# Kernel optimization log

Hardware: AMD Instinct MI355X
Metric: run time of the kernel (lower is better)

Reference implementation:

```python
import jax, jax.numpy as jnp
import numpy as np

GROUPS = 32
EPS = 1e-6


def group_norm(x, gamma, beta):
    b, c, h, w = x.shape
    xg = x.reshape(b, GROUPS, c // GROUPS, h, w)
    mu = xg.mean(axis=(2, 3, 4), keepdims=True)
    var = xg.var(axis=(2, 3, 4), keepdims=True)
    xn = ((xg - mu) * jax.lax.rsqrt(var + EPS)).reshape(b, c, h, w)
    return xn * gamma[None, :, None, None] + beta[None, :, None, None]


def conv1x1(x, w, b):
    # x: (b,c_in,h,w), w: (c_out,c_in), b: (c_out,)
    return jnp.einsum('oc,bchw->bohw', w, x) + b[None, :, None, None]


def setup_inputs() -> dict:
    key = jax.random.key(0)
    ks = jax.random.split(key, 10)
    c = 512
    scale = 1.0 / np.sqrt(c)
    inp = jax.random.normal(ks[0], (16, c, 32, 32), dtype=jnp.float32)
    return {
        'inp': inp,
        'gamma': jnp.ones((c,), jnp.float32),
        'beta': jnp.zeros((c,), jnp.float32),
        'Wq': jax.random.normal(ks[1], (c, c), jnp.float32) * scale,
        'bq': jnp.zeros((c,), jnp.float32),
        'Wk': jax.random.normal(ks[2], (c, c), jnp.float32) * scale,
        'bk': jnp.zeros((c,), jnp.float32),
        'Wv': jax.random.normal(ks[3], (c, c), jnp.float32) * scale,
        'bv': jnp.zeros((c,), jnp.float32),
        'Wo': jax.random.normal(ks[4], (c, c), jnp.float32) * scale,
        'bo': jnp.zeros((c,), jnp.float32),
    }


def reference(inp, gamma, beta, Wq, bq, Wk, bk, Wv, bv, Wo, bo):
    b, c, h, w = inp.shape
    x = group_norm(inp, gamma, beta)
    Q = conv1x1(x, Wq, bq).reshape(b, c, h * w)  # (b,c,n)
    K = conv1x1(x, Wk, bk).reshape(b, c, h * w)  # (b,c,m)
    V = conv1x1(x, Wv, bv).reshape(b, c, h * w)  # (b,c,m)
    # attn[b,n,m] = sum_c Q[b,c,n] * K[b,c,m], scaled then softmax over m
    attn = jnp.einsum('bcn,bcm->bnm', Q, K) / jnp.sqrt(jnp.float32(c))
    attn = jax.nn.softmax(attn, axis=2)
    # A[b,c,n] = sum_m V[b,c,m] * attn[b,n,m]  (== bmm(V, attn^T))
    A = jnp.einsum('bcm,bnm->bcn', V, attn).reshape(b, c, h, w)
    A = conv1x1(A, Wo, bo)
    return inp + A
```

## Files before the change

kernel.cpp:

```cpp
#include <hip/hip_runtime.h>

typedef unsigned short UST;
typedef __attribute__((ext_vector_type(8))) short bf16x8;
typedef __attribute__((ext_vector_type(8))) unsigned short us8;
typedef __attribute__((ext_vector_type(4))) float f32x4;

__device__ __forceinline__ UST f2bf(float f) {
  union { float f; unsigned int u; } x; x.f = f;
  unsigned int r = x.u + 0x7fffu + ((x.u >> 16) & 1u);
  return (UST)(r >> 16);
}
__device__ __forceinline__ float bf2f(UST h) {
  union { unsigned int u; float f; } x; x.u = ((unsigned int)h) << 16;
  return x.f;
}

__device__ __forceinline__ void sync_lds() {
  asm volatile("s_waitcnt lgkmcnt(0)\n\ts_barrier" ::: "memory");
}
__device__ __forceinline__ void barrier_nowait() {
  asm volatile("s_barrier" ::: "memory");
}

typedef const __attribute__((address_space(1))) void g_void;
typedef __attribute__((address_space(3))) void lds_void;
__device__ __forceinline__ void gload16(const UST* g, UST* l) {
  __builtin_amdgcn_global_load_lds((g_void*)g, (lds_void*)l, 16, 0, 0);
}

__global__ __launch_bounds__(256) void prep(
    const float* __restrict__ inp, const float* __restrict__ gamma,
    const float* __restrict__ beta, UST* __restrict__ Xnt,
    const float4* __restrict__ wq, const float4* __restrict__ wk,
    const float4* __restrict__ wv, const float4* __restrict__ wo,
    ushort4* __restrict__ oqkv, ushort4* __restrict__ owo,
    const float4* __restrict__ bq4, const float4* __restrict__ bk4,
    const float4* __restrict__ bv4, float4* __restrict__ bqkv4,
    float4* __restrict__ l4) {
  const int tid = threadIdx.x;
  if (blockIdx.x >= 768) {
    int i = (blockIdx.x - 768) * 256 + tid;
    l4[i] = make_float4(0.f, 0.f, 0.f, 0.f);
    return;
  }
  if (blockIdx.x >= 512) {
    const int wb = blockIdx.x - 512;
    int i = wb * 256 + tid;
    float4 v;
    v = wq[i]; oqkv[i]          = make_ushort4(f2bf(v.x), f2bf(v.y), f2bf(v.z), f2bf(v.w));
    v = wk[i]; oqkv[i + 65536]  = make_ushort4(f2bf(v.x), f2bf(v.y), f2bf(v.z), f2bf(v.w));
    v = wv[i]; oqkv[i + 131072] = make_ushort4(f2bf(v.x), f2bf(v.y), f2bf(v.z), f2bf(v.w));
    v = wo[i]; owo[i]           = make_ushort4(f2bf(v.x), f2bf(v.y), f2bf(v.z), f2bf(v.w));
    if (wb < 2) {
      int t = wb * 256 + tid;
      if (t < 384) bqkv4[t] = (t < 128) ? bq4[t] : (t < 256 ? bk4[t - 128] : bv4[t - 256]);
    }
    return;
  }
  const int g = blockIdx.x & 31, b = blockIdx.x >> 5;
  const float4* p4 = (const float4*)(inp + ((size_t)b * 32 + g) * 16384);
  float x[16][4];
  float s = 0.f, ss = 0.f;
#pragma unroll
  for (int i = 0; i < 16; i++) {
    float4 t = p4[tid + i * 256];
    x[i][0] = t.x; x[i][1] = t.y; x[i][2] = t.z; x[i][3] = t.w;
    s += t.x + t.y + t.z + t.w;
    ss += t.x * t.x + t.y * t.y + t.z * t.z + t.w * t.w;
  }
  for (int o = 32; o >= 1; o >>= 1) { s += __shfl_xor(s, o); ss += __shfl_xor(ss, o); }
  __shared__ float red[8];
  __shared__ float mu_s, rstd_s;
  const int w = tid >> 6;
  if ((tid & 63) == 0) { red[w * 2] = s; red[w * 2 + 1] = ss; }
  __syncthreads();
  if (tid == 0) {
    float S1 = red[0] + red[2] + red[4] + red[6];
    float S2 = red[1] + red[3] + red[5] + red[7];
    float mu = S1 * (1.f / 16384.f);
    float var = S2 * (1.f / 16384.f) - mu * mu;
    mu_s = mu; rstd_s = rsqrtf(var + 1e-6f);
  }
  __syncthreads();
  const float mu = mu_s, rstd = rstd_s;
#pragma unroll
  for (int o2 = 0; o2 < 2; o2++) {
    const int ccg = g * 2 + o2;
    float sc[8], sh[8];
#pragma unroll
    for (int j = 0; j < 8; j++) {
      int ch = ccg * 8 + j;
      sc[j] = gamma[ch] * rstd;
      sh[j] = beta[ch] - mu * sc[j];
    }
#pragma unroll
    for (int m = 0; m < 4; m++) {
      us8 v;
#pragma unroll
      for (int j = 0; j < 8; j++) v[j] = f2bf(x[o2 * 8 + j][m] * sc[j] + sh[j]);
      *(us8*)(Xnt + (size_t)b * 524288 + (size_t)ccg * 8192 + (size_t)(4 * tid + m) * 8) = v;
    }
  }
}

template <int EPI, int NT, int AR, int BR>
__global__ __launch_bounds__(256, 4) void gemm_bt(
    const UST* __restrict__ A, const UST* __restrict__ B, void* __restrict__ C,
    const float* __restrict__ bias, const float* __restrict__ extra, float scale,
    int K, int ldc,
    int rsA, int csA, int ssA, int rsB, int csB, int ssB,
    long zA, long zB, long zC) {
  __shared__ __align__(16) UST buf[16384];

  const int tid = threadIdx.x;
  int m0, n0, z;
  if constexpr (NT > 0) {
    int lin = blockIdx.x + NT * (blockIdx.y + gridDim.y * blockIdx.z);
    int T = gridDim.y * gridDim.z;
    int per = T >> 3;
    int g = lin & 7, idx = lin >> 3;
    int at = g * per + idx / NT;
    int x = idx % NT;
    m0 = (at % gridDim.y) * 128; z = at / gridDim.y; n0 = x * 128;
  } else {
    m0 = blockIdx.y * 128; n0 = blockIdx.x * 128; z = blockIdx.z;
  }
  const UST* Ab = A + (long)z * zA;
  const UST* Bb = B + (long)z * zB;

  const int w = tid >> 6, lane = tid & 63;
  const int quad = lane >> 4, l16 = lane & 15;
  const int wm = w >> 1, wn = w & 1;

  f32x4 acc[4][4];
#pragma unroll
  for (int i = 0; i < 4; i++)
#pragma unroll
    for (int j = 0; j < 4; j++) acc[i][j] = f32x4{0.f, 0.f, 0.f, 0.f};

  const UST* gA[2];
  const UST* gB[2];
#pragma unroll
  for (int t = 0; t < 2; t++) {
    int q = t * 256 + w * 64 + lane;
    int row, kc;
    if constexpr (AR) { kc = q >> 7; row = q & 127; }
    else {
      row = q >> 2; int kk = q & 3;
      kc = kk ^ (((row >> 1) ^ (row >> 3)) & 3);
    }
    gA[t] = Ab + (size_t)(m0 + row) * rsA + (size_t)kc * csA;
  }
#pragma unroll
  for (int t = 0; t < 2; t++) {
    int q = t * 256 + w * 64 + lane;
    int row, kc;
    if constexpr (BR) { kc = q >> 7; row = q & 127; }
    else {
      row = q >> 2; int kk = q & 3;
      kc = kk ^ (((row >> 1) ^ (row >> 3)) & 3);
    }
    gB[t] = Bb + (size_t)(n0 + row) * rsB + (size_t)kc * csB;
  }
  int aoff[4], boff[4];
#pragma unroll
  for (int i = 0; i < 4; i++) {
    int R = wm * 64 + i * 16 + l16;
    if constexpr (AR) aoff[i] = quad * 1024 + R * 8;
    else {
      int s = ((R >> 1) ^ (R >> 3)) & 3;
      aoff[i] = R * 32 + (quad ^ s) * 8;
    }
  }
#pragma unroll
  for (int j = 0; j < 4; j++) {
    int R = wn * 64 + j * 16 + l16;
    if constexpr (BR) boff[j] = quad * 1024 + R * 8;
    else {
      int s = ((R >> 1) ^ (R >> 3)) & 3;
      boff[j] = R * 32 + (quad ^ s) * 8;
    }
  }

  const int nk = K >> 5;

#define STAGE(bb)                                   \
  {                                                 \
    UST* sA = buf + (bb) * 8192;                    \
    UST* sB = sA + 4096;                            \
    _Pragma("unroll") for (int t = 0; t < 2; t++) { \
      gload16(gA[t], sA + t * 2048 + w * 512);      \
      gA[t] += ssA;                                 \
    }                                               \
    _Pragma("unroll") for (int t = 0; t < 2; t++) { \
      gload16(gB[t], sB + t * 2048 + w * 512);      \
      gB[t] += ssB;                                 \
    }                                               \
  }

  STAGE(0)
  STAGE(1)

  for (int k = 0; k < nk; ++k) {
    if (k + 1 < nk) asm volatile("s_waitcnt vmcnt(4)" ::: "memory");
    else            asm volatile("s_waitcnt vmcnt(0)" ::: "memory");
    barrier_nowait();
    const UST* cA = buf + (k & 1) * 8192;
    const UST* cB = cA + 4096;
    bf16x8 af[4], bfr[4];
#pragma unroll
    for (int i = 0; i < 4; i++) af[i] = *(const bf16x8*)(cA + aoff[i]);
#pragma unroll
    for (int j = 0; j < 4; j++) bfr[j] = *(const bf16x8*)(cB + boff[j]);
    __builtin_amdgcn_s_setprio(1);
#pragma unroll
    for (int i = 0; i < 4; i++)
#pragma unroll
      for (int j = 0; j < 4; j++)
        acc[i][j] = __builtin_amdgcn_mfma_f32_16x16x32_bf16(af[i], bfr[j], acc[i][j], 0, 0, 0);
    __builtin_amdgcn_s_setprio(0);
    if (k + 2 < nk) {
      sync_lds();
      STAGE(k & 1)
    }
  }
  sync_lds();

  if constexpr (EPI == 4) {
    float* fbuf = (float*)buf;
    float* Cb = (float*)C + (long)z * zC;
    const float* Eb = extra + (long)z * zC;
#pragma unroll
    for (int p = 0; p < 4; ++p) {
      if (p) barrier_nowait();
      if (wm == (p >> 1)) {
#pragma unroll
        for (int ii = 0; ii < 2; ii++) {
          const int i = (p & 1) * 2 + ii;
#pragma unroll
          for (int j = 0; j < 4; j++)
#pragma unroll
            for (int r = 0; r < 4; r++)
              fbuf[(ii * 16 + quad * 4 + r) * 132 + wn * 64 + j * 16 + l16] = acc[i][j][r];
        }
      }
      sync_lds();
#pragma unroll
      for (int it = 0; it < 4; ++it) {
        int q = tid + it * 256;
        int row = q >> 5, colc = q & 31;
        int gr = m0 + p * 32 + row;
        size_t off = (size_t)gr * ldc + n0 + colc * 4;
        float4 v = *(float4*)&fbuf[row * 132 + colc * 4];
        float4 e = *(const float4*)&Eb[off];
        float bb = bias[gr];
        v.x += bb + e.x; v.y += bb + e.y; v.z += bb + e.z; v.w += bb + e.w;
        *(float4*)&Cb[off] = v;
      }
    }
  } else if constexpr (EPI == 7) {
    UST* Cb = (UST*)C + (long)z * zC;
    float* lrow = (float*)extra + (long)z * 1024;
#pragma unroll
    for (int h = 0; h < 2; ++h) {
      if (h) barrier_nowait();
      if (wm == h) {
#pragma unroll
        for (int i = 0; i < 4; i++)
#pragma unroll
          for (int j = 0; j < 4; j++)
#pragma unroll
            for (int r = 0; r < 4; r++) {
              float v = __expf(acc[i][j][r] * scale);
              buf[(i * 16 + quad * 4 + r) * 136 + wn * 64 + j * 16 + l16] = f2bf(v);
            }
      }
      sync_lds();
#pragma unroll
      for (int it = 0; it < 4; ++it) {
        int q = tid + it * 256;
        int row = q >> 4, colc = q & 15;
        us8 v = *(us8*)&buf[row * 136 + colc * 8];
        *(us8*)&Cb[(size_t)(m0 + h * 64 + row) * ldc + n0 + colc * 8] = v;
        float s = 0.f;
#pragma unroll
        for (int j = 0; j < 8; j++) s += bf2f(v[j]);
        s += __shfl_xor(s, 8); s += __shfl_xor(s, 4);
        s += __shfl_xor(s, 2); s += __shfl_xor(s, 1);
        if ((lane & 15) == 0) atomicAdd(&lrow[m0 + h * 64 + row], s);
      }
    }
  } else if constexpr (EPI == 8) {
    UST* Cb = (UST*)C + (long)z * zC;
    const float* lrow = bias + (long)z * 1024;
#pragma unroll
    for (int h = 0; h < 2; ++h) {
      if (h) barrier_nowait();
      if (wm == h) {
#pragma unroll
        for (int i = 0; i < 4; i++) {
          float rs[4];
#pragma unroll
          for (int r = 0; r < 4; r++)
            rs[r] = 1.0f / lrow[m0 + h * 64 + i * 16 + quad * 4 + r];
#pragma unroll
          for (int j = 0; j < 4; j++)
#pragma unroll
            for (int r = 0; r < 4; r++)
              buf[(i * 16 + quad * 4 + r) * 136 + wn * 64 + j * 16 + l16] =
                  f2bf(acc[i][j][r] * rs[r]);
        }
      }
      sync_lds();
#pragma unroll
      for (int it = 0; it < 4; ++it) {
        int q = tid + it * 256;
        int row = q >> 4, colc = q & 15;
        us8 v = *(us8*)&buf[row * 136 + colc * 8];
        *(us8*)&Cb[(size_t)(m0 + h * 64 + row) * ldc + n0 + colc * 8] = v;
      }
    }
  } else {
    const bool vreg = (n0 >= 1024);
    if (!vreg) {
      UST* Cb = (UST*)C + (long)z * zC;
#pragma unroll
      for (int h = 0; h < 2; ++h) {
        if (h) barrier_nowait();
        if (wm == h) {
#pragma unroll
          for (int i = 0; i < 4; i++)
#pragma unroll
            for (int j = 0; j < 4; j++) {
              const float bc = bias[n0 + wn * 64 + j * 16 + l16];
#pragma unroll
              for (int r = 0; r < 4; r++)
                buf[(i * 16 + quad * 4 + r) * 136 + wn * 64 + j * 16 + l16] =
                    f2bf(acc[i][j][r] + bc);
            }
        }
        sync_lds();
#pragma unroll
        for (int it = 0; it < 4; ++it) {
          int q = tid + it * 256;
          int row = q >> 4, colc = q & 15;
          us8 v = *(us8*)&buf[row * 136 + colc * 8];
          *(us8*)&Cb[(size_t)(m0 + h * 64 + row) * ldc + n0 + colc * 8] = v;
        }
      }
    } else {
      UST* Vb = (UST*)extra + (long)z * 524288;
#pragma unroll
      for (int h = 0; h < 2; ++h) {
        if (h) barrier_nowait();
        if (wn == h) {
#pragma unroll
          for (int i = 0; i < 4; i++)
#pragma unroll
            for (int j = 0; j < 4; j++) {
              const float bc = bias[n0 + wn * 64 + j * 16 + l16];
              ushort4 sv;
              sv.x = f2bf(acc[i][j][0] + bc);
              sv.y = f2bf(acc[i][j][1] + bc);
              sv.z = f2bf(acc[i][j][2] + bc);
              sv.w = f2bf(acc[i][j][3] + bc);
              *(ushort4*)&buf[(j * 16 + l16) * 136 + wm * 64 + i * 16 + quad * 4] = sv;
            }
        }
        sync_lds();
#pragma unroll
        for (int it = 0; it < 4; ++it) {
          int q = tid + it * 256;
          int c = q >> 4, mc = q & 15;
          us8 v = *(us8*)&buf[c * 136 + mc * 8];
          *(us8*)&Vb[(size_t)(n0 - 1024 + h * 64 + c) * 1024 + m0 + mc * 8] = v;
        }
      }
    }
  }
#undef STAGE
}

extern "C" void kernel_launch(void* const* d_in, const int* in_sizes, int n_in,
                              void* d_out, int out_size, void* d_ws, size_t ws_size,
                              hipStream_t stream) {
  const float* inp   = (const float*)d_in[0];
  const float* gamma = (const float*)d_in[1];
  const float* beta  = (const float*)d_in[2];
  const float* Wq    = (const float*)d_in[3];
  const float* bq    = (const float*)d_in[4];
  const float* Wk    = (const float*)d_in[5];
  const float* bk    = (const float*)d_in[6];
  const float* Wv    = (const float*)d_in[7];
  const float* bv    = (const float*)d_in[8];
  const float* Wo    = (const float*)d_in[9];
  const float* bo    = (const float*)d_in[10];
  float* out = (float*)d_out;
  char* ws = (char*)d_ws;

  UST*   Xnt   = (UST*)(ws);
  UST*   QKt   = (UST*)(ws + ((size_t)16 << 20));
  UST*   V     = (UST*)(ws + ((size_t)48 << 20));
  UST*   P     = (UST*)(ws + ((size_t)64 << 20));
  float* bqkv  = (float*)(ws + ((size_t)96 << 20));
  UST*   Wqkvb = (UST*)(ws + ((size_t)96 << 20) + 8192);
  UST*   Wob   = Wqkvb + 786432;
  float* l     = (float*)(ws + ((size_t)100 << 20));
  UST*   At    = Xnt;

  prep<<<784, 256, 0, stream>>>(
      inp, gamma, beta, Xnt,
      (const float4*)Wq, (const float4*)Wk, (const float4*)Wv, (const float4*)Wo,
      (ushort4*)Wqkvb, (ushort4*)Wob,
      (const float4*)bq, (const float4*)bk, (const float4*)bv, (float4*)bqkv,
      (float4*)l);

  gemm_bt<6, 12, 1, 0><<<dim3(12, 8, 16), 256, 0, stream>>>(
      Xnt, Wqkvb, QKt, bqkv, (const float*)V, 1.f,
      512, 1024, 8, 8192, 32768, 512, 8, 32, 524288, 0, 1048576);
  gemm_bt<7, 8, 0, 0><<<dim3(8, 8, 16), 256, 0, stream>>>(
      QKt, QKt + 512, P, nullptr, (const float*)l, 0.04419417382415922f,
      512, 1024, 1024, 8, 32, 1024, 8, 32, 1048576, 1048576, 1048576);
  gemm_bt<8, 4, 0, 0><<<dim3(4, 8, 16), 256, 0, stream>>>(
      P, V, At, (const float*)l, nullptr, 1.f,
      1024, 512, 1024, 8, 32, 1024, 8, 32, 1048576, 524288, 524288);
  gemm_bt<4, 8, 0, 0><<<dim3(8, 4, 16), 256, 0, stream>>>(
      Wob, At, out, bo, inp, 1.f,
      512, 1024, 512, 8, 32, 512, 8, 32, 0, 524288, 524288);
}
```

Measured before the change: 213.4 us.

## Add 256x256-tile 8-wave GEMM with phased prefetch for QKV and QK^T

Adds a new gemm8p kernel: 512 threads, 256x256 output tiles, a 128 KB double-buffered LDS and a four-phase ping-pong schedule. In each phase, MFMA work overlaps the global-to-LDS staging of the next K slice, with explicit vmcnt waits and setprio. The QKV projection and the exp(QK^T) score GEMM now use it, with their epilogues moved over; the gemm_bt variants lose those epilogues. The larger tiles are meant to raise data reuse per loaded byte and hide load latency. In exchange, fewer blocks are launched (384 and 256) and register/LDS pressure is high, which limits occupancy.

```diff
diff --git a/kernel.cpp b/kernel.cpp
--- a/kernel.cpp
+++ b/kernel.cpp
@@ -103,6 +103,233 @@
   }
 }
 
+template <int EPI, int NT, int AR>
+__global__ __launch_bounds__(512, 2) void gemm8p(
+    const UST* __restrict__ A, const UST* __restrict__ B, void* __restrict__ C,
+    const float* __restrict__ bias, const float* __restrict__ extra, float scale,
+    int K, int ldc, int rsA, int csA, long ssA, int rsB, long ssB,
+    long zA, long zB, long zC) {
+  __shared__ __align__(16) UST buf[65536];
+
+  const int tid = threadIdx.x;
+  int lin = blockIdx.x + NT * (blockIdx.y + gridDim.y * blockIdx.z);
+  int T = gridDim.y * gridDim.z;
+  int per = T >> 3;
+  int g = lin & 7, idx = lin >> 3;
+  int at = g * per + idx / NT;
+  int x = idx % NT;
+  const int m0 = (at % gridDim.y) * 256;
+  const int z = at / gridDim.y;
+  const int n0 = x * 256;
+
+  const UST* Ab = A + (long)z * zA;
+  const UST* Bb = B + (long)z * zB;
+
+  const int w = tid >> 6, lane = tid & 63;
+  const int quad = lane >> 4, l16 = lane & 15;
+  const int wr = w >> 2, wc = w & 3;
+
+  f32x4 acc[8][4];
+#pragma unroll
+  for (int i = 0; i < 8; i++)
+#pragma unroll
+    for (int j = 0; j < 4; j++) acc[i][j] = f32x4{0.f, 0.f, 0.f, 0.f};
+
+  const UST* gp[8];
+  int lo[8];
+  {
+    const int lr = w * 8 + (lane >> 3);
+    const int kcl = (lane & 7) ^ (lane >> 3);
+#pragma unroll
+    for (int p = 0; p < 8; p++) {
+      int q;
+      bool isA;
+      if (p == 0) { q = 0; isA = true; }
+      else if (p == 1) { q = 2; isA = true; }
+      else if (p == 6) { q = 1; isA = true; }
+      else if (p == 7) { q = 3; isA = true; }
+      else { q = p - 2; isA = false; }
+      if (isA) {
+        if (AR) gp[p] = Ab + (size_t)(m0 + q * 64 + lane) * rsA + (size_t)w * csA;
+        else    gp[p] = Ab + (size_t)(m0 + q * 64 + lr) * rsA + (size_t)kcl * csA;
+        lo[p] = q * 4096 + w * 512;
+      } else {
+        gp[p] = Bb + (size_t)(n0 + q * 64 + lr) * rsB + (size_t)kcl * 8;
+        lo[p] = 16384 + q * 4096 + w * 512;
+      }
+    }
+  }
+
+  int aoffs[8][2], boffs[4][2];
+#pragma unroll
+  for (int i = 0; i < 8; i++) {
+    int R = wr * 128 + i * 16 + l16;
+    int q = R >> 6, lr = R & 63;
+#pragma unroll
+    for (int ks = 0; ks < 2; ks++) {
+      int kc = ks * 4 + quad;
+      aoffs[i][ks] = AR ? (q * 4096 + (kc * 64 + lr) * 8)
+                        : (q * 4096 + (lr * 8 + (kc ^ (lr & 7))) * 8);
+    }
+  }
+#pragma unroll
+  for (int j = 0; j < 4; j++) {
+    int R = wc * 64 + j * 16 + l16;
+    int q = R >> 6, lr = R & 63;
+#pragma unroll
+    for (int ks = 0; ks < 2; ks++) {
+      int kc = ks * 4 + quad;
+      boffs[j][ks] = 16384 + q * 4096 + (lr * 8 + (kc ^ (lr & 7))) * 8;
+    }
+  }
+
+  const int nk = K >> 6;
+
+#define STG(P, SS) { gload16(gp[P], lb + lo[P]); gp[P] += (SS); }
+
+  {
+    UST* lb = buf;
+    STG(0, ssA) STG(1, ssA) STG(2, ssB) STG(3, ssB)
+    STG(4, ssB) STG(5, ssB) STG(6, ssA) STG(7, ssA)
+  }
+  asm volatile("s_waitcnt vmcnt(2)" ::: "memory");
+  barrier_nowait();
+
+#define PH(IH, JH, P0, P1, SS0, SS1, VME)                                     \
+  {                                                                           \
+    bf16x8 af[4][2], bfr[2][2];                                               \
+    _Pragma("unroll") for (int il = 0; il < 4; il++)                          \
+      _Pragma("unroll") for (int ks = 0; ks < 2; ks++)                        \
+        af[il][ks] = *(const bf16x8*)(cb + aoffs[(IH)*4 + il][ks]);           \
+    _Pragma("unroll") for (int jl = 0; jl < 2; jl++)                          \
+      _Pragma("unroll") for (int ks = 0; ks < 2; ks++)                        \
+        bfr[jl][ks] = *(const bf16x8*)(cb + boffs[(JH)*2 + jl][ks]);          \
+    if (stg) { STG(P0, SS0) STG(P1, SS1) }                                    \
+    barrier_nowait();                                                         \
+    asm volatile("s_waitcnt lgkmcnt(0)" ::: "memory");                        \
+    __builtin_amdgcn_sched_barrier(0);                                        \
+    __builtin_amdgcn_s_setprio(1);                                            \
+    _Pragma("unroll") for (int il = 0; il < 4; il++)                          \
+      _Pragma("unroll") for (int jl = 0; jl < 2; jl++)                        \
+        _Pragma("unroll") for (int ks = 0; ks < 2; ks++)                      \
+          acc[(IH)*4 + il][(JH)*2 + jl] = __builtin_amdgcn_mfma_f32_16x16x32_bf16( \
+              af[il][ks], bfr[jl][ks], acc[(IH)*4 + il][(JH)*2 + jl], 0, 0, 0);    \
+    __builtin_amdgcn_s_setprio(0);                                            \
+    VME;                                                                      \
+    barrier_nowait();                                                         \
+  }
+
+  for (int t = 0; t < nk; ++t) {
+    const UST* cb = buf + (t & 1) * 32768;
+    UST* lb = buf + ((t + 1) & 1) * 32768;
+    const bool stg = (t + 1 < nk);
+    PH(0, 0, 0, 1, ssA, ssA, {})
+    PH(0, 1, 2, 3, ssB, ssB, {
+      if (stg) { asm volatile("s_waitcnt vmcnt(4)" ::: "memory"); }
+      else     { asm volatile("s_waitcnt vmcnt(0)" ::: "memory"); }
+    })
+    PH(1, 0, 4, 5, ssB, ssB, {})
+    PH(1, 1, 6, 7, ssA, ssA, {
+      if (stg) { asm volatile("s_waitcnt vmcnt(2)" ::: "memory"); }
+    })
+  }
+#undef PH
+#undef STG
+
+  if constexpr (EPI == 7) {
+    UST* Cb = (UST*)C + (long)z * zC;
+    float* lrow = (float*)extra + (long)z * 1024;
+#pragma unroll
+    for (int h = 0; h < 2; ++h) {
+      if (h) barrier_nowait();
+      if (wr == h) {
+#pragma unroll
+        for (int i = 0; i < 8; i++)
+#pragma unroll
+          for (int j = 0; j < 4; j++)
+#pragma unroll
+            for (int r = 0; r < 4; r++) {
+              float v = __expf(acc[i][j][r] * scale);
+              buf[(i * 16 + quad * 4 + r) * 260 + wc * 64 + j * 16 + l16] = f2bf(v);
+            }
+      }
+      sync_lds();
+#pragma unroll
+      for (int it = 0; it < 8; ++it) {
+        int q = tid + it * 512;
+        int row = q >> 5, colc = q & 31;
+        us8 v = *(us8*)&buf[row * 260 + colc * 8];
+        *(us8*)&Cb[(size_t)(m0 + h * 128 + row) * ldc + n0 + colc * 8] = v;
+        float s = 0.f;
+#pragma unroll
+        for (int jj = 0; jj < 8; jj++) s += bf2f(v[jj]);
+        s += __shfl_xor(s, 16); s += __shfl_xor(s, 8);
+        s += __shfl_xor(s, 4); s += __shfl_xor(s, 2); s += __shfl_xor(s, 1);
+        if ((lane & 31) == 0) atomicAdd(&lrow[m0 + h * 128 + row], s);
+      }
+    }
+  } else {
+    const bool vreg = (n0 >= 1024);
+    if (!vreg) {
+      UST* Cb = (UST*)C + (long)z * zC;
+#pragma unroll
+      for (int h = 0; h < 2; ++h) {
+        if (h) barrier_nowait();
+        if (wr == h) {
+#pragma unroll
+          for (int i = 0; i < 8; i++)
+#pragma unroll
+            for (int j = 0; j < 4; j++) {
+              const float bc = bias[n0 + wc * 64 + j * 16 + l16];
+#pragma unroll
+              for (int r = 0; r < 4; r++)
+                buf[(i * 16 + quad * 4 + r) * 260 + wc * 64 + j * 16 + l16] =
+                    f2bf(acc[i][j][r] + bc);
+            }
+        }
+        sync_lds();
+#pragma unroll
+        for (int it = 0; it < 8; ++it) {
+          int q = tid + it * 512;
+          int row = q >> 5, colc = q & 31;
+          us8 v = *(us8*)&buf[row * 260 + colc * 8];
+          *(us8*)&Cb[(size_t)(m0 + h * 128 + row) * ldc + n0 + colc * 8] = v;
+        }
+      }
+    } else {
+      UST* Vb = (UST*)extra + (long)z * 524288;
+#pragma unroll
+      for (int h = 0; h < 2; ++h) {
+        if (h) barrier_nowait();
+        if ((wc >> 1) == h) {
+#pragma unroll
+          for (int i = 0; i < 8; i++)
+#pragma unroll
+            for (int j = 0; j < 4; j++) {
+              const float bc = bias[n0 + wc * 64 + j * 16 + l16];
+              const int Cl = (wc & 1) * 64 + j * 16 + l16;
+              const int R0 = wr * 128 + i * 16 + quad * 4;
+              ushort4 sv;
+              sv.x = f2bf(acc[i][j][0] + bc);
+              sv.y = f2bf(acc[i][j][1] + bc);
+              sv.z = f2bf(acc[i][j][2] + bc);
+              sv.w = f2bf(acc[i][j][3] + bc);
+              *(ushort4*)&buf[Cl * 260 + R0] = sv;
+            }
+        }
+        sync_lds();
+#pragma unroll
+        for (int it = 0; it < 8; ++it) {
+          int q = tid + it * 512;
+          int Cl = q >> 5, mc = q & 31;
+          us8 v = *(us8*)&buf[Cl * 260 + mc * 8];
+          *(us8*)&Vb[(size_t)(n0 - 1024 + h * 128 + Cl) * 1024 + m0 + mc * 8] = v;
+        }
+      }
+    }
+  }
+}
+
 template <int EPI, int NT, int AR, int BR>
 __global__ __launch_bounds__(256, 4) void gemm_bt(
     const UST* __restrict__ A, const UST* __restrict__ B, void* __restrict__ C,
@@ -258,22 +485,26 @@
         *(float4*)&Cb[off] = v;
       }
     }
-  } else if constexpr (EPI == 7) {
+  } else if constexpr (EPI == 8) {
     UST* Cb = (UST*)C + (long)z * zC;
-    float* lrow = (float*)extra + (long)z * 1024;
+    const float* lrow = bias + (long)z * 1024;
 #pragma unroll
     for (int h = 0; h < 2; ++h) {
       if (h) barrier_nowait();
       if (wm == h) {
 #pragma unroll
-        for (int i = 0; i < 4; i++)
+        for (int i = 0; i < 4; i++) {
+          float rs[4];
+#pragma unroll
+          for (int r = 0; r < 4; r++)
+            rs[r] = 1.0f / lrow[m0 + h * 64 + i * 16 + quad * 4 + r];
 #pragma unroll
           for (int j = 0; j < 4; j++)
 #pragma unroll
-            for (int r = 0; r < 4; r++) {
-              float v = __expf(acc[i][j][r] * scale);
-              buf[(i * 16 + quad * 4 + r) * 136 + wn * 64 + j * 16 + l16] = f2bf(v);
-            }
+            for (int r = 0; r < 4; r++)
+              buf[(i * 16 + quad * 4 + r) * 136 + wn * 64 + j * 16 + l16] =
+                  f2bf(acc[i][j][r] * rs[r]);
+        }
       }
       sync_lds();
 #pragma unroll
@@ -282,99 +513,6 @@
         int row = q >> 4, colc = q & 15;
         us8 v = *(us8*)&buf[row * 136 + colc * 8];
         *(us8*)&Cb[(size_t)(m0 + h * 64 + row) * ldc + n0 + colc * 8] = v;
-        float s = 0.f;
-#pragma unroll
-        for (int j = 0; j < 8; j++) s += bf2f(v[j]);
-        s += __shfl_xor(s, 8); s += __shfl_xor(s, 4);
-        s += __shfl_xor(s, 2); s += __shfl_xor(s, 1);
-        if ((lane & 15) == 0) atomicAdd(&lrow[m0 + h * 64 + row], s);
-      }
-    }
-  } else if constexpr (EPI == 8) {
-    UST* Cb = (UST*)C + (long)z * zC;
-    const float* lrow = bias + (long)z * 1024;
-#pragma unroll
-    for (int h = 0; h < 2; ++h) {
-      if (h) barrier_nowait();
-      if (wm == h) {
-#pragma unroll
-        for (int i = 0; i < 4; i++) {
-          float rs[4];
-#pragma unroll
-          for (int r = 0; r < 4; r++)
-            rs[r] = 1.0f / lrow[m0 + h * 64 + i * 16 + quad * 4 + r];
-#pragma unroll
-          for (int j = 0; j < 4; j++)
-#pragma unroll
-            for (int r = 0; r < 4; r++)
-              buf[(i * 16 + quad * 4 + r) * 136 + wn * 64 + j * 16 + l16] =
-                  f2bf(acc[i][j][r] * rs[r]);
-        }
-      }
-      sync_lds();
-#pragma unroll
-      for (int it = 0; it < 4; ++it) {
-        int q = tid + it * 256;
-        int row = q >> 4, colc = q & 15;
-        us8 v = *(us8*)&buf[row * 136 + colc * 8];
-        *(us8*)&Cb[(size_t)(m0 + h * 64 + row) * ldc + n0 + colc * 8] = v;
-      }
-    }
-  } else {
-    const bool vreg = (n0 >= 1024);
-    if (!vreg) {
-      UST* Cb = (UST*)C + (long)z * zC;
-#pragma unroll
-      for (int h = 0; h < 2; ++h) {
-        if (h) barrier_nowait();
-        if (wm == h) {
-#pragma unroll
-          for (int i = 0; i < 4; i++)
-#pragma unroll
-            for (int j = 0; j < 4; j++) {
-              const float bc = bias[n0 + wn * 64 + j * 16 + l16];
-#pragma unroll
-              for (int r = 0; r < 4; r++)
-                buf[(i * 16 + quad * 4 + r) * 136 + wn * 64 + j * 16 + l16] =
-                    f2bf(acc[i][j][r] + bc);
-            }
-        }
-        sync_lds();
-#pragma unroll
-        for (int it = 0; it < 4; ++it) {
-          int q = tid + it * 256;
-          int row = q >> 4, colc = q & 15;
-          us8 v = *(us8*)&buf[row * 136 + colc * 8];
-          *(us8*)&Cb[(size_t)(m0 + h * 64 + row) * ldc + n0 + colc * 8] = v;
-        }
-      }
-    } else {
-      UST* Vb = (UST*)extra + (long)z * 524288;
-#pragma unroll
-      for (int h = 0; h < 2; ++h) {
-        if (h) barrier_nowait();
-        if (wn == h) {
-#pragma unroll
-          for (int i = 0; i < 4; i++)
-#pragma unroll
-            for (int j = 0; j < 4; j++) {
-              const float bc = bias[n0 + wn * 64 + j * 16 + l16];
-              ushort4 sv;
-              sv.x = f2bf(acc[i][j][0] + bc);
-              sv.y = f2bf(acc[i][j][1] + bc);
-              sv.z = f2bf(acc[i][j][2] + bc);
-              sv.w = f2bf(acc[i][j][3] + bc);
-              *(ushort4*)&buf[(j * 16 + l16) * 136 + wm * 64 + i * 16 + quad * 4] = sv;
-            }
-        }
-        sync_lds();
-#pragma unroll
-        for (int it = 0; it < 4; ++it) {
-          int q = tid + it * 256;
-          int c = q >> 4, mc = q & 15;
-          us8 v = *(us8*)&buf[c * 136 + mc * 8];
-          *(us8*)&Vb[(size_t)(n0 - 1024 + h * 64 + c) * 1024 + m0 + mc * 8] = v;
-        }
       }
     }
   }
@@ -415,12 +553,12 @@
       (const float4*)bq, (const float4*)bk, (const float4*)bv, (float4*)bqkv,
       (float4*)l);
 
-  gemm_bt<6, 12, 1, 0><<<dim3(12, 8, 16), 256, 0, stream>>>(
+  gemm8p<6, 6, 1><<<dim3(6, 4, 16), 512, 0, stream>>>(
       Xnt, Wqkvb, QKt, bqkv, (const float*)V, 1.f,
-      512, 1024, 8, 8192, 32768, 512, 8, 32, 524288, 0, 1048576);
-  gemm_bt<7, 8, 0, 0><<<dim3(8, 8, 16), 256, 0, stream>>>(
+      512, 1024, 8, 8192, 65536, 512, 64, 524288, 0, 1048576);
+  gemm8p<7, 4, 0><<<dim3(4, 4, 16), 512, 0, stream>>>(
       QKt, QKt + 512, P, nullptr, (const float*)l, 0.04419417382415922f,
-      512, 1024, 1024, 8, 32, 1024, 8, 32, 1048576, 1048576, 1048576);
+      512, 1024, 1024, 8, 64, 1024, 64, 1048576, 1048576, 1048576);
   gemm_bt<8, 4, 0, 0><<<dim3(4, 8, 16), 256, 0, stream>>>(
       P, V, At, (const float*)l, nullptr, 1.f,
       1024, 512, 1024, 8, 32, 1024, 8, 32, 1048576, 524288, 524288);
```

Result: slower. 241.1 us (+13.0%).

## Fuse QK^T softmax and PV into one attention kernel with P kept in LDS

Applied to the files above, without the earlier changes.

Replaces the separate QK^T+exp GEMM and the P·V GEMM with a single attention kernel. Each 512-thread block computes exp scores for 64 queries against all 1024 keys, keeps the bf16 probabilities in 128KB of shared memory and reduces the row sums locally. It then multiplies by V and normalizes. This removes the global P buffer round trip, the atomicAdd row-sum reduction and the zeroing of l in prep. The cost is a large LDS footprint that limits residency to one block per CU, and Q/K/V operands are loaded straight from global memory without LDS staging, which may expose memory latency.

```diff
diff --git a/kernel.cpp b/kernel.cpp
--- a/kernel.cpp
+++ b/kernel.cpp
@@ -35,14 +35,8 @@
     const float4* __restrict__ wv, const float4* __restrict__ wo,
     ushort4* __restrict__ oqkv, ushort4* __restrict__ owo,
     const float4* __restrict__ bq4, const float4* __restrict__ bk4,
-    const float4* __restrict__ bv4, float4* __restrict__ bqkv4,
-    float4* __restrict__ l4) {
+    const float4* __restrict__ bv4, float4* __restrict__ bqkv4) {
   const int tid = threadIdx.x;
-  if (blockIdx.x >= 768) {
-    int i = (blockIdx.x - 768) * 256 + tid;
-    l4[i] = make_float4(0.f, 0.f, 0.f, 0.f);
-    return;
-  }
   if (blockIdx.x >= 512) {
     const int wb = blockIdx.x - 512;
     int i = wb * 256 + tid;
@@ -103,6 +97,177 @@
   }
 }
 
+__global__ __launch_bounds__(512, 2) void attn(
+    const UST* __restrict__ QKt, const UST* __restrict__ V,
+    UST* __restrict__ At, float scale) {
+  __shared__ __align__(16) UST Ps[65536];
+  __shared__ float lbuf[512];
+  __shared__ __align__(16) float linv[64];
+
+  const int tid = threadIdx.x;
+  const int lin = blockIdx.x;
+  const int b  = (lin & 7) * 2 + (lin >> 7);
+  const int n0 = ((lin >> 3) & 15) * 64;
+
+  const UST* qk = QKt + (size_t)b * 1048576;
+  const UST* vb = V   + (size_t)b * 524288;
+  UST* ob       = At  + (size_t)b * 524288 + (size_t)n0 * 512;
+
+  const int w = tid >> 6, lane = tid & 63;
+  const int quad = lane >> 4, l16 = lane & 15;
+  const int xr = (l16 & 7) << 2;
+
+  int qoff[4];
+#pragma unroll
+  for (int jn = 0; jn < 4; jn++)
+    qoff[jn] = (n0 + jn * 16 + l16) * 1024 + quad * 8;
+
+  float lp[4] = {0.f, 0.f, 0.f, 0.f};
+
+#define LDS1(KF, QF, KS)                                          \
+  _Pragma("unroll") for (int t = 0; t < 4; t++) {                 \
+    KF[t] = *(const bf16x8*)(qk + koff[t] + (KS) * 32);           \
+    QF[t] = *(const bf16x8*)(qk + qoff[t] + (KS) * 32);           \
+  }
+#define MM1(KF, QF)                                               \
+  __builtin_amdgcn_s_setprio(1);                                  \
+  _Pragma("unroll") for (int im = 0; im < 4; im++)                \
+    _Pragma("unroll") for (int jn = 0; jn < 4; jn++)              \
+      s[im][jn] = __builtin_amdgcn_mfma_f32_16x16x32_bf16(        \
+          KF[im], QF[jn], s[im][jn], 0, 0, 0);                    \
+  __builtin_amdgcn_s_setprio(0);
+
+#pragma unroll
+  for (int mg = 0; mg < 2; ++mg) {
+    int koff[4];
+#pragma unroll
+    for (int im = 0; im < 4; im++)
+      koff[im] = (w * 128 + mg * 64 + im * 16 + l16) * 1024 + 512 + quad * 8;
+
+    f32x4 s[4][4];
+#pragma unroll
+    for (int i = 0; i < 4; i++)
+#pragma unroll
+      for (int j = 0; j < 4; j++) s[i][j] = f32x4{0.f, 0.f, 0.f, 0.f};
+
+    bf16x8 kA[4], qA[4], kB[4], qB[4];
+    LDS1(kA, qA, 0)
+#pragma unroll
+    for (int ks2 = 0; ks2 < 8; ks2++) {
+      LDS1(kB, qB, 2 * ks2 + 1)
+      MM1(kA, qA)
+      if (ks2 < 7) { LDS1(kA, qA, 2 * ks2 + 2) }
+      MM1(kB, qB)
+    }
+
+#pragma unroll
+    for (int im = 0; im < 4; im++) {
+      const int chunk = w * 16 + mg * 8 + im * 2 + (quad >> 1);
+#pragma unroll
+      for (int jn = 0; jn < 4; jn++) {
+        ushort4 pv;
+        float e0 = __expf(s[im][jn][0] * scale);
+        float e1 = __expf(s[im][jn][1] * scale);
+        float e2 = __expf(s[im][jn][2] * scale);
+        float e3 = __expf(s[im][jn][3] * scale);
+        pv.x = f2bf(e0); pv.y = f2bf(e1); pv.z = f2bf(e2); pv.w = f2bf(e3);
+        lp[jn] += bf2f(pv.x) + bf2f(pv.y) + bf2f(pv.z) + bf2f(pv.w);
+        const int nl = jn * 16 + l16;
+        *(ushort4*)&Ps[nl * 1024 + (chunk ^ xr) * 8 + (quad & 1) * 4] = pv;
+      }
+    }
+  }
+#undef LDS1
+#undef MM1
+
+#pragma unroll
+  for (int jn = 0; jn < 4; jn++) {
+    lp[jn] += __shfl_xor(lp[jn], 16);
+    lp[jn] += __shfl_xor(lp[jn], 32);
+  }
+  if (quad == 0) {
+#pragma unroll
+    for (int jn = 0; jn < 4; jn++) lbuf[w * 64 + jn * 16 + l16] = lp[jn];
+  }
+  sync_lds();
+  if (tid < 64) {
+    float sa = 0.f;
+#pragma unroll
+    for (int ww = 0; ww < 8; ww++) sa += lbuf[ww * 64 + tid];
+    linv[tid] = 1.0f / sa;
+  }
+  sync_lds();
+
+  f32x4 o[4][4];
+#pragma unroll
+  for (int i = 0; i < 4; i++)
+#pragma unroll
+    for (int j = 0; j < 4; j++) o[i][j] = f32x4{0.f, 0.f, 0.f, 0.f};
+
+  int voff[4];
+#pragma unroll
+  for (int jc = 0; jc < 4; jc++)
+    voff[jc] = (w * 64 + jc * 16 + l16) * 1024 + quad * 8;
+  int pbase[4];
+#pragma unroll
+  for (int i = 0; i < 4; i++) pbase[i] = (i * 16 + l16) * 1024;
+
+#define LDV(VF, KS)                                               \
+  _Pragma("unroll") for (int t = 0; t < 4; t++)                   \
+    VF[t] = *(const bf16x8*)(vb + voff[t] + (KS) * 32);
+#define LDP(PF, KS)                                               \
+  _Pragma("unroll") for (int t = 0; t < 4; t++)                   \
+    PF[t] = *(const bf16x8*)&Ps[pbase[t] + ((((KS) * 4 + quad) ^ xr) << 3)];
+#define MM2(PF, VF)                                               \
+  __builtin_amdgcn_s_setprio(1);                                  \
+  _Pragma("unroll") for (int i = 0; i < 4; i++)                   \
+    _Pragma("unroll") for (int jc = 0; jc < 4; jc++)              \
+      o[i][jc] = __builtin_amdgcn_mfma_f32_16x16x32_bf16(         \
+          PF[i], VF[jc], o[i][jc], 0, 0, 0);                      \
+  __builtin_amdgcn_s_setprio(0);
+
+  {
+    bf16x8 vA[4], vB[4];
+    LDV(vA, 0)
+#pragma unroll
+    for (int ks2 = 0; ks2 < 16; ks2++) {
+      bf16x8 pA[4], pB[4];
+      LDP(pA, 2 * ks2)
+      LDV(vB, 2 * ks2 + 1)
+      MM2(pA, vA)
+      LDP(pB, 2 * ks2 + 1)
+      if (ks2 < 15) { LDV(vA, 2 * ks2 + 2) }
+      MM2(pB, vB)
+    }
+  }
+#undef LDV
+#undef LDP
+#undef MM2
+
+  sync_lds();
+  f32x4 li[4];
+#pragma unroll
+  for (int i = 0; i < 4; i++) li[i] = *(f32x4*)&linv[i * 16 + quad * 4];
+
+  UST* obuf = Ps;
+#pragma unroll
+  for (int i = 0; i < 4; i++)
+#pragma unroll
+    for (int jc = 0; jc < 4; jc++)
+#pragma unroll
+      for (int r = 0; r < 4; r++)
+        obuf[(i * 16 + quad * 4 + r) * 520 + w * 64 + jc * 16 + l16] =
+            f2bf(o[i][jc][r] * li[i][r]);
+  sync_lds();
+#pragma unroll
+  for (int it = 0; it < 8; ++it) {
+    int q = tid + it * 512;
+    int row = q >> 6, cc = q & 63;
+    us8 vv = *(us8*)&obuf[row * 520 + cc * 8];
+    *(us8*)&ob[(size_t)row * 512 + cc * 8] = vv;
+  }
+}
+
 template <int EPI, int NT, int AR, int BR>
 __global__ __launch_bounds__(256, 4) void gemm_bt(
     const UST* __restrict__ A, const UST* __restrict__ B, void* __restrict__ C,
@@ -256,68 +421,6 @@
         float bb = bias[gr];
         v.x += bb + e.x; v.y += bb + e.y; v.z += bb + e.z; v.w += bb + e.w;
         *(float4*)&Cb[off] = v;
-      }
-    }
-  } else if constexpr (EPI == 7) {
-    UST* Cb = (UST*)C + (long)z * zC;
-    float* lrow = (float*)extra + (long)z * 1024;
-#pragma unroll
-    for (int h = 0; h < 2; ++h) {
-      if (h) barrier_nowait();
-      if (wm == h) {
-#pragma unroll
-        for (int i = 0; i < 4; i++)
-#pragma unroll
-          for (int j = 0; j < 4; j++)
-#pragma unroll
-            for (int r = 0; r < 4; r++) {
-              float v = __expf(acc[i][j][r] * scale);
-              buf[(i * 16 + quad * 4 + r) * 136 + wn * 64 + j * 16 + l16] = f2bf(v);
-            }
-      }
-      sync_lds();
-#pragma unroll
-      for (int it = 0; it < 4; ++it) {
-        int q = tid + it * 256;
-        int row = q >> 4, colc = q & 15;
-        us8 v = *(us8*)&buf[row * 136 + colc * 8];
-        *(us8*)&Cb[(size_t)(m0 + h * 64 + row) * ldc + n0 + colc * 8] = v;
-        float s = 0.f;
-#pragma unroll
-        for (int j = 0; j < 8; j++) s += bf2f(v[j]);
-        s += __shfl_xor(s, 8); s += __shfl_xor(s, 4);
-        s += __shfl_xor(s, 2); s += __shfl_xor(s, 1);
-        if ((lane & 15) == 0) atomicAdd(&lrow[m0 + h * 64 + row], s);
-      }
-    }
-  } else if constexpr (EPI == 8) {
-    UST* Cb = (UST*)C + (long)z * zC;
-    const float* lrow = bias + (long)z * 1024;
-#pragma unroll
-    for (int h = 0; h < 2; ++h) {
-      if (h) barrier_nowait();
-      if (wm == h) {
-#pragma unroll
-        for (int i = 0; i < 4; i++) {
-          float rs[4];
-#pragma unroll
-          for (int r = 0; r < 4; r++)
-            rs[r] = 1.0f / lrow[m0 + h * 64 + i * 16 + quad * 4 + r];
-#pragma unroll
-          for (int j = 0; j < 4; j++)
-#pragma unroll
-            for (int r = 0; r < 4; r++)
-              buf[(i * 16 + quad * 4 + r) * 136 + wn * 64 + j * 16 + l16] =
-                  f2bf(acc[i][j][r] * rs[r]);
-        }
-      }
-      sync_lds();
-#pragma unroll
-      for (int it = 0; it < 4; ++it) {
-        int q = tid + it * 256;
-        int row = q >> 4, colc = q & 15;
-        us8 v = *(us8*)&buf[row * 136 + colc * 8];
-        *(us8*)&Cb[(size_t)(m0 + h * 64 + row) * ldc + n0 + colc * 8] = v;
       }
     }
   } else {
@@ -401,29 +504,21 @@
   UST*   Xnt   = (UST*)(ws);
   UST*   QKt   = (UST*)(ws + ((size_t)16 << 20));
   UST*   V     = (UST*)(ws + ((size_t)48 << 20));
-  UST*   P     = (UST*)(ws + ((size_t)64 << 20));
   float* bqkv  = (float*)(ws + ((size_t)96 << 20));
   UST*   Wqkvb = (UST*)(ws + ((size_t)96 << 20) + 8192);
   UST*   Wob   = Wqkvb + 786432;
-  float* l     = (float*)(ws + ((size_t)100 << 20));
   UST*   At    = Xnt;
 
-  prep<<<784, 256, 0, stream>>>(
+  prep<<<768, 256, 0, stream>>>(
       inp, gamma, beta, Xnt,
       (const float4*)Wq, (const float4*)Wk, (const float4*)Wv, (const float4*)Wo,
       (ushort4*)Wqkvb, (ushort4*)Wob,
-      (const float4*)bq, (const float4*)bk, (const float4*)bv, (float4*)bqkv,
-      (float4*)l);
+      (const float4*)bq, (const float4*)bk, (const float4*)bv, (float4*)bqkv);
 
   gemm_bt<6, 12, 1, 0><<<dim3(12, 8, 16), 256, 0, stream>>>(
       Xnt, Wqkvb, QKt, bqkv, (const float*)V, 1.f,
       512, 1024, 8, 8192, 32768, 512, 8, 32, 524288, 0, 1048576);
-  gemm_bt<7, 8, 0, 0><<<dim3(8, 8, 16), 256, 0, stream>>>(
-      QKt, QKt + 512, P, nullptr, (const float*)l, 0.04419417382415922f,
-      512, 1024, 1024, 8, 32, 1024, 8, 32, 1048576, 1048576, 1048576);
-  gemm_bt<8, 4, 0, 0><<<dim3(4, 8, 16), 256, 0, stream>>>(
-      P, V, At, (const float*)l, nullptr, 1.f,
-      1024, 512, 1024, 8, 32, 1024, 8, 32, 1048576, 524288, 524288);
+  attn<<<256, 512, 0, stream>>>(QKt, V, At, 0.04419417382415922f);
   gemm_bt<4, 8, 0, 0><<<dim3(8, 4, 16), 256, 0, stream>>>(
       Wob, At, out, bo, inp, 1.f,
       512, 1024, 512, 8, 32, 512, 8, 32, 0, 524288, 524288);
```

After: 251.1 us. 1.18x slower.
